# Kernel tuning notes

Hardware: AMD Instinct MI355X
Metric: run time of the kernel (lower is better)

The kernel has to match this reference:

```python
import jax, jax.numpy as jnp
import numpy as np

NUM_CLASSES = 40
EOS_COEF = 0.1
IGNORE = 255
W_CLASS, W_MASK, W_DICE = 2.0, 5.0, 5.0
EPS = 1e-8


def setup_inputs() -> dict:
    key = jax.random.key(0)
    k1, k2, k3, k4 = jax.random.split(key, 4)
    B, Q, H, W = 4, 100, 256, 256
    pred_logits = jax.random.normal(k1, (B, Q, NUM_CLASSES + 1), dtype=jnp.float32)
    pred_masks = jax.random.normal(k2, (B, Q, H, W), dtype=jnp.float32)
    targets = jax.random.randint(k3, (B, H, W), 0, NUM_CLASSES)
    ign = jax.random.uniform(k4, (B, H, W)) < 0.05
    targets = jnp.where(ign, IGNORE, targets).astype(jnp.int32)
    return {"pred_logits": pred_logits, "pred_masks": pred_masks, "targets": targets}


def reference(pred_logits, pred_masks, targets):
    B, Q, _ = pred_logits.shape
    C = NUM_CLASSES
    f32 = jnp.float32
    valid = targets != IGNORE                      # [B,H,W]
    tgt_safe = jnp.where(valid, targets, 0)        # in-range for indexing

    # ---- loss_labels: pixel->query assignment, per-query mode label ----
    # sigmoid is monotone, so argmax over queries of raw logits == argmax of sigmoid
    assign = jnp.argmax(pred_masks, axis=1)        # [B,H,W]
    b_idx = jnp.broadcast_to(jnp.arange(B)[:, None, None], targets.shape)
    # counts[b,q,c] = #valid pixels assigned to query q with label c
    counts = jnp.zeros((B, Q, C), f32).at[b_idx, assign, tgt_safe].add(valid.astype(f32))
    has_pix = counts.sum(-1) > 0                   # [B,Q]
    # mode = argmax of counts (ties -> smallest class, matching torch.mode)
    target_classes = jnp.where(has_pix, jnp.argmax(counts, axis=-1), C)  # [B,Q]

    logp = jax.nn.log_softmax(pred_logits, axis=-1)                      # [B,Q,C+1]
    nll = -jnp.take_along_axis(logp, target_classes[..., None], axis=-1)[..., 0]
    empty_weight = jnp.ones(C + 1, f32).at[-1].set(EOS_COEF)
    # ignore_index = num_classes in the CE over classes
    ce = jnp.where(target_classes != C, nll * empty_weight[target_classes], 0.0)
    p = jnp.exp(-ce)
    loss_ce = jnp.mean((1.0 - p) ** 2 * ce)

    # ---- loss_masks: per-pixel CE over queries + per-class dice ----
    logp_pix = jax.nn.log_softmax(pred_masks, axis=1)                    # [B,Q,H,W]
    nll_pix = -jnp.take_along_axis(logp_pix, tgt_safe[:, None], axis=1)[:, 0]  # [B,H,W]
    n_valid = valid.astype(f32).sum()
    ce_mask = jnp.sum(jnp.where(valid, nll_pix, 0.0)) / jnp.maximum(n_valid, 1.0)

    sig = jax.nn.sigmoid(pred_masks)                                     # [B,Q,H,W]
    tmask = (targets[:, None] == jnp.arange(C)[None, :, None, None]).astype(f32)  # [B,C,H,W]
    vm = valid[:, None].astype(f32)                                      # [B,1,H,W]
    inter = jnp.einsum('bqhw,bchw->bqc', sig, tmask * vm)                # numerator uses valid mask
    src_sum = sig.sum(axis=(2, 3))                                       # [B,Q]
    tsum = tmask.sum(axis=(2, 3))                                        # [B,C]
    dice = 2.0 * inter / (src_sum[:, :, None] + tsum[:, None, :] + EPS)  # [B,Q,C]
    present = tsum.sum(axis=0) > 0                                       # [C]
    dice_loss = jnp.sum(jnp.where(present, 1.0 - dice.mean(axis=(0, 1)), 0.0)) / C

    combined = W_MASK * ce_mask + W_DICE * dice_loss
    return W_CLASS * loss_ce + combined
```

## Files before the change

kernel.cpp:

```cpp
#include <hip/hip_runtime.h>

constexpr int B = 4, Q = 100, C = 40, Cp1 = 41, HW = 65536;

constexpr int FBLKS = 512;

constexpr int WS_WORDS = 32562;

typedef __attribute__((ext_vector_type(8))) short short8;
typedef __attribute__((ext_vector_type(4))) float f32x4;

__device__ __forceinline__ short f2bf(float f) {
    unsigned u = __float_as_uint(f);
    u += 0x7FFF + ((u >> 16) & 1);
    return (short)(u >> 16);
}

__device__ __forceinline__ void gload16(const void* g, void* l) {
    __builtin_amdgcn_global_load_lds(
        (const __attribute__((address_space(1))) unsigned*)g,
        (__attribute__((address_space(3))) unsigned*)l, 16, 0, 0);
}

__global__ void kZ(unsigned* __restrict__ ws, int n) {
    int i = blockIdx.x * blockDim.x + threadIdx.x;
    for (; i < n; i += gridDim.x * blockDim.x) ws[i] = 0u;
}

__global__ __launch_bounds__(256) void kF(const float* __restrict__ masks,
                                          const int* __restrict__ targets,
                                          unsigned* __restrict__ counts,
                                          unsigned* __restrict__ tsum,
                                          float* __restrict__ ce_sum,
                                          unsigned* __restrict__ n_valid,
                                          float* __restrict__ inter_ext) {
    __shared__ __align__(16) float stageF[16 * 512];
    __shared__ __align__(16) short tileS[2][16 * 512];
    __shared__ __align__(8) unsigned char tgt8[512];
    __shared__ unsigned ts_local[C];
    __shared__ float cred[4];
    __shared__ unsigned vred[4];

    const int tid = threadIdx.x;
    const int l = tid & 63, w = tid >> 6;
    const int m = l & 15, quad = l >> 4;

    const int blk = blockIdx.x;
    const int b = blk >> 7;
    const int seg = blk & 127;
    const int p0 = seg * 512 + 2 * tid;

    const int2 tg = *(const int2*)(targets + (size_t)b * HW + p0);
    const int tg0 = tg.x, tg1 = tg.y;
    *(unsigned short*)&tgt8[2 * tid] =
        (unsigned short)((tg0 & 255) | ((tg1 & 255) << 8));
    if (tid < C) ts_local[tid] = 0u;

    const float* mseg = masks + (size_t)b * Q * HW + seg * 512;

    auto STAGE = [&](int qt) {
        const int q0 = qt * 16 + w * 4;
        if (q0 < 100) {
            const float* pb = mseg + (size_t)q0 * HW;
            char* lb = (char*)stageF + (w * 4) * 2048;
            #pragma unroll
            for (int j = 0; j < 8; ++j) {
                const int u = j >> 1, half = j & 1;
                gload16(pb + (size_t)u * HW + half * 256 + l * 4,
                        lb + u * 2048 + half * 1024);
            }
        }
    };

    STAGE(0);

    float m20 = -INFINITY, m21 = -INFINITY;
    float s0 = 0.f, s1 = 0.f, xt0 = 0.f, xt1 = 0.f;
    int am0 = 0, am1 = 0;

    const int cv = (w == 2 && m == 8) ? 255 : (w * 16 + m);

    for (int qt = 0; qt < 7; ++qt) {
        char* tbq = (char*)(&tileS[qt & 1][0]);
        const int nu = (qt == 6) ? 4 : 16;

        __syncthreads();

        #pragma unroll
        for (int u = 0; u < 16; ++u)
            if (u < nu) {
                const int q = qt * 16 + u;
                const float2 vp = *(const float2*)&stageF[u * 512 + 2 * tid];
                const float v0 = vp.x, v1 = vp.y;
                s0 += __expf(v0);
                s1 += __expf(v1);
                am0 = (v0 > m20) ? q : am0;  m20 = fmaxf(m20, v0);
                am1 = (v1 > m21) ? q : am1;  m21 = fmaxf(m21, v1);
                xt0 = (q == tg0) ? v0 : xt0;
                xt1 = (q == tg1) ? v1 : xt1;
                const float g0 = __builtin_amdgcn_rcpf(1.f + __expf(-v0));
                const float g1 = __builtin_amdgcn_rcpf(1.f + __expf(-v1));
                const unsigned pk = (unsigned)(unsigned short)f2bf(g0) |
                                    ((unsigned)(unsigned short)f2bf(g1) << 16);
                *(unsigned*)(tbq + ((u * 1024 + 4 * tid) ^ ((u & 7) << 4))) = pk;
            }

        __syncthreads();

        if (qt < 6) STAGE(qt + 1);

        if (w < 3) {
            f32x4 acc = {0.f, 0.f, 0.f, 0.f};
            #pragma unroll
            for (int kc = 0; kc < 16; ++kc) {
                const short8 av = *(const short8*)(tbq +
                    ((m * 1024 + kc * 64 + quad * 16) ^ ((m & 7) << 4)));
                const unsigned long long tw =
                    *(const unsigned long long*)&tgt8[kc * 32 + quad * 8];
                short8 bv;
                #pragma unroll
                for (int j = 0; j < 8; ++j)
                    bv[j] = ((int)((tw >> (8 * j)) & 255) == cv)
                                ? (short)0x3F80 : (short)0;
                acc = __builtin_amdgcn_mfma_f32_16x16x32_bf16(av, bv, acc,
                                                              0, 0, 0);
            }
            if (!(w == 2 && m > 8)) {
                #pragma unroll
                for (int reg = 0; reg < 4; ++reg) {
                    const int q = qt * 16 + quad * 4 + reg;
                    if (q < 100)
                        atomicAdd(&inter_ext[(size_t)(b * Q + q) * Cp1 +
                                             w * 16 + m], acc[reg]);
                }
            }
        }
    }

    float ce = 0.f;
    unsigned nv = 0u;
    if (tg0 != 255) {
        ce += __logf(s0) - xt0; nv++;
        atomicAdd(&counts[((size_t)b * Q + am0) * C + tg0], 1u);
        atomicAdd(&ts_local[tg0], 1u);
    }
    if (tg1 != 255) {
        ce += __logf(s1) - xt1; nv++;
        atomicAdd(&counts[((size_t)b * Q + am1) * C + tg1], 1u);
        atomicAdd(&ts_local[tg1], 1u);
    }
    for (int off = 32; off; off >>= 1) {
        ce += __shfl_xor(ce, off);
        nv += __shfl_xor(nv, off);
    }
    if (l == 0) { cred[w] = ce; vred[w] = nv; }
    __syncthreads();
    if (tid == 0) {
        atomicAdd(ce_sum, cred[0] + cred[1] + cred[2] + cred[3]);
        atomicAdd(n_valid, vred[0] + vred[1] + vred[2] + vred[3]);
    }
    if (tid < C) {
        unsigned t = ts_local[tid];
        if (t) atomicAdd(&tsum[b * C + tid], t);
    }
}

__global__ __launch_bounds__(1024) void kC(const float* __restrict__ logits,
                                           const unsigned* __restrict__ counts,
                                           const unsigned* __restrict__ tsum,
                                           const float* __restrict__ inter_ext,
                                           const float* __restrict__ ce_sum,
                                           const unsigned* __restrict__ n_valid,
                                           float* __restrict__ out) {
    int tid = threadIdx.x;
    __shared__ float dice_sum[C];
    __shared__ float ssum[B * Q];
    __shared__ float wred[16];
    __shared__ float s_lce;
    if (tid < C) dice_sum[tid] = 0.f;
    if (tid < B * Q) {
        const float* r = inter_ext + (size_t)tid * Cp1;
        float t = 0.f;
        #pragma unroll
        for (int c = 0; c < Cp1; ++c) t += r[c];
        ssum[tid] = t;
    }

    float ce_acc = 0.f;
    for (int i = tid; i < B * Q; i += 1024) {
        const unsigned* cnt = counts + (size_t)i * C;
        unsigned best = 0;
        int tc = C;
        #pragma unroll
        for (int c = 0; c < C; ++c) {
            unsigned v = cnt[c];
            if (v > best) { best = v; tc = c; }
        }
        if (tc != C) {
            const float* lg = logits + (size_t)i * Cp1;
            float mm = -INFINITY, xt = 0.f;
            #pragma unroll
            for (int c = 0; c < Cp1; ++c) {
                float v = lg[c];
                mm = fmaxf(mm, v);
                if (c == tc) xt = v;
            }
            float ss = 0.f;
            #pragma unroll
            for (int c = 0; c < Cp1; ++c) ss += __expf(lg[c] - mm);
            float nll = mm + __logf(ss) - xt;
            float p = __expf(-nll);
            float om = 1.f - p;
            ce_acc += om * om * nll;
        }
    }
    for (int off = 32; off; off >>= 1) ce_acc += __shfl_xor(ce_acc, off);
    if ((tid & 63) == 0) wred[tid >> 6] = ce_acc;
    __syncthreads();
    if (tid == 0) {
        float t = 0.f;
        for (int w = 0; w < 16; ++w) t += wred[w];
        s_lce = t;
    }

    for (int i = tid; i < B * Q * C; i += 1024) {
        int bq = i / C, c = i - bq * C;
        float denom = ssum[bq] + (float)tsum[(bq / Q) * C + c] + 1e-8f;
        atomicAdd(&dice_sum[c], 2.f * inter_ext[(size_t)bq * Cp1 + c] / denom);
    }
    __syncthreads();

    if (tid == 0) {
        float dl = 0.f;
        for (int c = 0; c < C; ++c) {
            unsigned ts = tsum[c] + tsum[C + c] + tsum[2 * C + c] + tsum[3 * C + c];
            if (ts > 0) dl += 1.f - dice_sum[c] * (1.f / (B * Q));
        }
        dl *= (1.f / C);
        float ce_mask = ce_sum[0] / fmaxf((float)n_valid[0], 1.f);
        float lce = s_lce * (1.f / (B * Q));
        out[0] = 2.f * lce + 5.f * ce_mask + 5.f * dl;
    }
}

extern "C" void kernel_launch(void* const* d_in, const int* in_sizes, int n_in,
                              void* d_out, int out_size, void* d_ws, size_t ws_size,
                              hipStream_t stream) {
    const float* logits  = (const float*)d_in[0];
    const float* masks   = (const float*)d_in[1];
    const int*   targets = (const int*)d_in[2];
    float* out = (float*)d_out;

    unsigned* ws        = (unsigned*)d_ws;
    unsigned* counts    = ws;
    unsigned* tsum      = ws + 16000;
    float*    ce_sum    = (float*)(ws + 16160);
    unsigned* n_valid   = ws + 16161;
    float*    inter_ext = (float*)(ws + 16162);

    kZ<<<64, 256, 0, stream>>>(ws, WS_WORDS);
    kF<<<FBLKS, 256, 0, stream>>>(masks, targets, counts, tsum, ce_sum, n_valid,
                                  inter_ext);
    kC<<<1, 1024, 0, stream>>>(logits, counts, tsum, inter_ext, ce_sum, n_valid, out);
}
```

Before: 213.9 us.

## Split single-block finalize into per-row wave kernel plus tiny final reduction

The single 1024-thread finalize block is replaced by a kernel with one 64-lane wave per (batch, query) row. Each wave computes the row sum, dice contributions, mode class and focal CE using shuffles, and accumulates them with global atomics. A second one-wave kernel then combines the results into the scalar loss. This spreads the serial per-thread loops over many CUs, at the cost of an extra kernel launch and global atomic contention on 40 dice slots.

```diff
diff --git a/kernel.cpp b/kernel.cpp
--- a/kernel.cpp
+++ b/kernel.cpp
@@ -4,7 +4,7 @@
 
 constexpr int FBLKS = 512;
 
-constexpr int WS_WORDS = 32562;
+constexpr int WS_WORDS = 32603;
 
 typedef __attribute__((ext_vector_type(8))) short short8;
 typedef __attribute__((ext_vector_type(4))) float f32x4;
@@ -164,80 +164,77 @@
     }
 }
 
-__global__ __launch_bounds__(1024) void kC(const float* __restrict__ logits,
-                                           const unsigned* __restrict__ counts,
-                                           const unsigned* __restrict__ tsum,
-                                           const float* __restrict__ inter_ext,
-                                           const float* __restrict__ ce_sum,
-                                           const unsigned* __restrict__ n_valid,
-                                           float* __restrict__ out) {
-    int tid = threadIdx.x;
-    __shared__ float dice_sum[C];
-    __shared__ float ssum[B * Q];
-    __shared__ float wred[16];
-    __shared__ float s_lce;
-    if (tid < C) dice_sum[tid] = 0.f;
-    if (tid < B * Q) {
-        const float* r = inter_ext + (size_t)tid * Cp1;
-        float t = 0.f;
+__global__ __launch_bounds__(64) void kCrow(const float* __restrict__ logits,
+                                            const unsigned* __restrict__ counts,
+                                            const unsigned* __restrict__ tsum,
+                                            const float* __restrict__ inter_ext,
+                                            float* __restrict__ dice_g,
+                                            float* __restrict__ lce_acc) {
+    const int bq = blockIdx.x;
+    const int b = bq / Q;
+    const int l = threadIdx.x;
+
+    const float iv = (l < Cp1) ? inter_ext[(size_t)bq * Cp1 + l] : 0.f;
+    float ssum = iv;
+    #pragma unroll
+    for (int off = 32; off; off >>= 1) ssum += __shfl_xor(ssum, off);
+    if (l < C) {
+        const float denom = ssum + (float)tsum[b * C + l] + 1e-8f;
+        atomicAdd(&dice_g[l], 2.f * iv / denom);
+    }
+
+    const unsigned v = (l < C) ? counts[(size_t)bq * C + l] : 0u;
+    unsigned mx = v;
+    #pragma unroll
+    for (int off = 32; off; off >>= 1) {
+        const unsigned o = __shfl_xor(mx, off);
+        mx = (o > mx) ? o : mx;
+    }
+    int cand = (v == mx) ? l : 64;
+    #pragma unroll
+    for (int off = 32; off; off >>= 1) {
+        const int o = __shfl_xor(cand, off);
+        cand = (o < cand) ? o : cand;
+    }
+
+    if (mx != 0u) {
+        const int tc = cand;
+        const float x = (l < Cp1) ? logits[(size_t)bq * Cp1 + l] : -INFINITY;
+        float mm = x;
         #pragma unroll
-        for (int c = 0; c < Cp1; ++c) t += r[c];
-        ssum[tid] = t;
-    }
-
-    float ce_acc = 0.f;
-    for (int i = tid; i < B * Q; i += 1024) {
-        const unsigned* cnt = counts + (size_t)i * C;
-        unsigned best = 0;
-        int tc = C;
+        for (int off = 32; off; off >>= 1) mm = fmaxf(mm, __shfl_xor(mm, off));
+        float ss = (l < Cp1) ? __expf(x - mm) : 0.f;
         #pragma unroll
-        for (int c = 0; c < C; ++c) {
-            unsigned v = cnt[c];
-            if (v > best) { best = v; tc = c; }
+        for (int off = 32; off; off >>= 1) ss += __shfl_xor(ss, off);
+        const float xt = __shfl(x, tc);
+        if (l == 0) {
+            const float nll = mm + __logf(ss) - xt;
+            const float p = __expf(-nll);
+            const float om = 1.f - p;
+            atomicAdd(lce_acc, om * om * nll);
         }
-        if (tc != C) {
-            const float* lg = logits + (size_t)i * Cp1;
-            float mm = -INFINITY, xt = 0.f;
-            #pragma unroll
-            for (int c = 0; c < Cp1; ++c) {
-                float v = lg[c];
-                mm = fmaxf(mm, v);
-                if (c == tc) xt = v;
-            }
-            float ss = 0.f;
-            #pragma unroll
-            for (int c = 0; c < Cp1; ++c) ss += __expf(lg[c] - mm);
-            float nll = mm + __logf(ss) - xt;
-            float p = __expf(-nll);
-            float om = 1.f - p;
-            ce_acc += om * om * nll;
-        }
-    }
-    for (int off = 32; off; off >>= 1) ce_acc += __shfl_xor(ce_acc, off);
-    if ((tid & 63) == 0) wred[tid >> 6] = ce_acc;
-    __syncthreads();
-    if (tid == 0) {
-        float t = 0.f;
-        for (int w = 0; w < 16; ++w) t += wred[w];
-        s_lce = t;
-    }
-
-    for (int i = tid; i < B * Q * C; i += 1024) {
-        int bq = i / C, c = i - bq * C;
-        float denom = ssum[bq] + (float)tsum[(bq / Q) * C + c] + 1e-8f;
-        atomicAdd(&dice_sum[c], 2.f * inter_ext[(size_t)bq * Cp1 + c] / denom);
-    }
-    __syncthreads();
-
-    if (tid == 0) {
-        float dl = 0.f;
-        for (int c = 0; c < C; ++c) {
-            unsigned ts = tsum[c] + tsum[C + c] + tsum[2 * C + c] + tsum[3 * C + c];
-            if (ts > 0) dl += 1.f - dice_sum[c] * (1.f / (B * Q));
-        }
-        dl *= (1.f / C);
-        float ce_mask = ce_sum[0] / fmaxf((float)n_valid[0], 1.f);
-        float lce = s_lce * (1.f / (B * Q));
+    }
+}
+
+__global__ __launch_bounds__(64) void kCfin(const unsigned* __restrict__ tsum,
+                                            const float* __restrict__ dice_g,
+                                            const float* __restrict__ ce_sum,
+                                            const unsigned* __restrict__ n_valid,
+                                            const float* __restrict__ lce_acc,
+                                            float* __restrict__ out) {
+    const int l = threadIdx.x;
+    float dterm = 0.f;
+    if (l < C) {
+        const unsigned ts = tsum[l] + tsum[C + l] + tsum[2 * C + l] +
+                            tsum[3 * C + l];
+        if (ts > 0) dterm = 1.f - dice_g[l] * (1.f / (B * Q));
+    }
+    #pragma unroll
+    for (int off = 32; off; off >>= 1) dterm += __shfl_xor(dterm, off);
+    if (l == 0) {
+        const float dl = dterm * (1.f / C);
+        const float ce_mask = ce_sum[0] / fmaxf((float)n_valid[0], 1.f);
+        const float lce = lce_acc[0] * (1.f / (B * Q));
         out[0] = 2.f * lce + 5.f * ce_mask + 5.f * dl;
     }
 }
@@ -256,9 +253,13 @@
     float*    ce_sum    = (float*)(ws + 16160);
     unsigned* n_valid   = ws + 16161;
     float*    inter_ext = (float*)(ws + 16162);
+    float*    dice_g    = (float*)(ws + 32562);
+    float*    lce_acc   = (float*)(ws + 32602);
 
     kZ<<<64, 256, 0, stream>>>(ws, WS_WORDS);
     kF<<<FBLKS, 256, 0, stream>>>(masks, targets, counts, tsum, ce_sum, n_valid,
                                   inter_ext);
-    kC<<<1, 1024, 0, stream>>>(logits, counts, tsum, inter_ext, ce_sum, n_valid, out);
-}
+    kCrow<<<B * Q, 64, 0, stream>>>(logits, counts, tsum, inter_ext, dice_g,
+                                    lce_acc);
+    kCfin<<<1, 64, 0, stream>>>(tsum, dice_g, ce_sum, n_valid, lce_acc, out);
+}
```

Result: faster. 198.0 us (-7.4%).
